# Optimization experiments

Measured on AMD Instinct MI355X. Metric: run time of the kernel, lower is better.

The kernel has to match this reference:

```python
import jax, jax.numpy as jnp
import numpy as np

B, N, D, E, H = 16, 1024, 1024, 4, 16


def setup_inputs() -> dict:
    key = jax.random.key(0)
    k1, k2, k3, k4 = jax.random.split(key, 4)
    return {
        "input_tokens": jax.random.normal(k1, (B, N, D), dtype=jnp.float32),
        "expert_mask": jax.random.randint(k2, (B, N), 0, E, dtype=jnp.int32),
        "qkv_w": jax.random.normal(k3, (3 * D, D), dtype=jnp.float32) * 0.02,
        "proj_w": jax.random.normal(k4, (D, D), dtype=jnp.float32) * 0.02,
        "proj_b": jnp.zeros((D,), dtype=jnp.float32),
    }


def reference(input_tokens, expert_mask, qkv_w, proj_w, proj_b):
    b, n, d = input_tokens.shape
    hd = d // H
    scale = 1.0 / np.sqrt(hd).astype(np.float32)
    # nested expert e uses first d_e = D / 2^(E-1-e) features (expert E-1 = full dim)
    d_tok = d // (2 ** (E - 1 - expert_mask))                     # [B, N]
    feat_mask = (jnp.arange(d)[None, None, :] < d_tok[..., None]).astype(input_tokens.dtype)  # [B, N, D]
    # NestedLinearExpand: slice input features per token (== mask), full 3D output
    x_in = input_tokens * feat_mask
    qkv = jnp.einsum('bnd,fd->bnf', x_in, qkv_w).reshape(b, n, 3, H, hd)
    q, k, v = jnp.moveaxis(qkv, 2, 0)                             # each [B, N, H, hd]
    q = q.transpose(0, 2, 1, 3)                                   # [B, H, N, hd]
    k = k.transpose(0, 2, 1, 3)
    v = v.transpose(0, 2, 1, 3)
    scores = jnp.einsum('bhqd,bhkd->bhqk', q, k) * scale          # [B, H, N, N]
    attn = jax.nn.softmax(scores, axis=-1)
    x = jnp.einsum('bhqk,bhkd->bhqd', attn, v)                    # [B, H, N, hd]
    x = x.transpose(0, 2, 1, 3).reshape(b, n, d)
    # NestedLinearContract: full-dim matmul, only first d_e outputs kept per token
    y = jnp.einsum('bnd,fd->bnf', x, proj_w) + proj_b
    return y * feat_mask
```

## Files before the change

### kernel.cpp

```cpp
#include <hip/hip_runtime.h>
#include <hip/hip_bf16.h>


typedef __bf16 bf16_t;
typedef __bf16 bf16x8 __attribute__((ext_vector_type(8)));
typedef __bf16 bf16x4 __attribute__((ext_vector_type(4)));
typedef float f32x4 __attribute__((ext_vector_type(4)));
typedef float f32x16 __attribute__((ext_vector_type(16)));
typedef int i32x4 __attribute__((ext_vector_type(4)));

typedef __attribute__((address_space(1))) void gvoid;
typedef __attribute__((address_space(3))) void lvoid;

#define MFMA16(a, b, c) __builtin_amdgcn_mfma_f32_16x16x32_bf16((a), (b), (c), 0, 0, 0)
#define MFMA32(a, b, c) __builtin_amdgcn_mfma_f32_32x32x16_bf16((a), (b), (c), 0, 0, 0)
#define GLOAD_LDS16(gsrc, ldst) \
  __builtin_amdgcn_global_load_lds((gvoid*)(gsrc), (lvoid*)(ldst), 16, 0, 0)

#define QSCALE 0.18033688f

__device__ __forceinline__ unsigned cvtpk(float lo, float hi) {
  unsigned r;
  asm("v_cvt_pk_bf16_f32 %0, %1, %2" : "=v"(r) : "v"(lo), "v"(hi));
  return r;
}
__device__ __forceinline__ void pl32swap(unsigned& x, unsigned& y) {
  asm("v_permlane32_swap_b32 %0, %1" : "+v"(x), "+v"(y));
}

__global__ __launch_bounds__(256) void sort_batch(
    const int* __restrict__ em, int* __restrict__ perm, int* __restrict__ ems) {
  __shared__ int cnt[4], base[4], cur[4];
  const int b = blockIdx.x, t = threadIdx.x;
  if (t < 4) cnt[t] = 0;
  __syncthreads();
  int e[4];
#pragma unroll
  for (int i = 0; i < 4; ++i) {
    e[i] = em[b * 1024 + t * 4 + i];
    atomicAdd(&cnt[e[i]], 1);
  }
  __syncthreads();
  if (t == 0) {
    base[0] = 0; base[1] = cnt[0];
    base[2] = cnt[0] + cnt[1]; base[3] = cnt[0] + cnt[1] + cnt[2];
    cur[0] = cur[1] = cur[2] = cur[3] = 0;
  }
  __syncthreads();
#pragma unroll
  for (int i = 0; i < 4; ++i) {
    const int pos = base[e[i]] + atomicAdd(&cur[e[i]], 1);
    perm[b * 1024 + pos] = t * 4 + i;
    ems[b * 1024 + pos] = e[i];
  }
}

__global__ __launch_bounds__(256) void prep_tokens(
    const float* __restrict__ x, const int* __restrict__ perm,
    const int* __restrict__ ems, bf16_t* __restrict__ xq) {
  const int prow = blockIdx.x;
  const int orig = (prow & ~1023) + perm[prow];
  const int dt = 128 << ems[prow];
  const int d = threadIdx.x * 4;
  float4 v = ((const float4*)(x + (size_t)orig * 1024))[threadIdx.x];
  const bool keep = d < dt;
  bf16x4 o;
  o[0] = (bf16_t)(keep ? v.x : 0.f);
  o[1] = (bf16_t)(keep ? v.y : 0.f);
  o[2] = (bf16_t)(keep ? v.z : 0.f);
  o[3] = (bf16_t)(keep ? v.w : 0.f);
  *((bf16x4*)(xq + (size_t)prow * 1024 + d)) = o;
}

__global__ __launch_bounds__(256) void conv_w(
    const float* __restrict__ s, bf16_t* __restrict__ dvec) {
  const int i = blockIdx.x * 256 + threadIdx.x;
  float4 v = ((const float4*)s)[i];
  bf16x4 o;
  o[0] = (bf16_t)v.x; o[1] = (bf16_t)v.y; o[2] = (bf16_t)v.z; o[3] = (bf16_t)v.w;
  ((bf16x4*)dvec)[i] = o;
}

template <int EPI>
__global__ __launch_bounds__(512, 2) void gemm256(
    const bf16_t* __restrict__ A, const bf16_t* __restrict__ Bw, int K,
    const int* __restrict__ perm, const int* __restrict__ ems,
    bf16_t* __restrict__ qo, bf16_t* __restrict__ ko, bf16_t* __restrict__ vto,
    float* __restrict__ yout, const float* __restrict__ bias) {
  __shared__ bf16_t lds[2][32768];
  const int tid = threadIdx.x;
  const int lane = tid & 63, w = tid >> 6;
  const int wm = w >> 2, wn = w & 3;
  const int g = lane >> 4, c16 = lane & 15;

  const int bid = blockIdx.x;
  const int rowbase = (bid & 63) * 256;
  const int colbase = (bid >> 6) * 256;

  const int dtmax = 128 << ems[rowbase + 255];

  if constexpr (EPI == 1) {
    if (colbase >= dtmax) {
      const float4 z = make_float4(0.f, 0.f, 0.f, 0.f);
#pragma unroll
      for (int i = 0; i < 32; ++i) {
        const int idx = i * 512 + tid;
        const int r = idx >> 6, c4 = idx & 63;
        const int orow = ((rowbase + r) & ~1023) + perm[rowbase + r];
        ((float4*)(yout + (size_t)orow * 1024 + colbase))[c4] = z;
      }
      return;
    }
  }

  const int NT = (EPI == 0) ? (dtmax >> 6) : (K >> 6);

  const int trow = tid >> 3;
  const int scol = (((tid & 7) ^ (trow & 7)) << 3);
  const bf16_t* pa = A + (size_t)(rowbase + trow) * K + scol;
  const bf16_t* pb = Bw + (size_t)(colbase + trow) * K + scol;

#define STAGE(j, koff, dst)                                       \
  GLOAD_LDS16(((j) < 4 ? pa + (size_t)((j) * 64) * K              \
                       : pb + (size_t)(((j) - 4) * 64) * K) +     \
                  (koff),                                         \
              (dst) + ((j) * 512 + tid) * 8)

#define LDFRAG(base, R, kk)            \
  (*(const bf16x8*)((base) + (size_t)(R) * 64 + \
                    (((((kk) << 2) + g) ^ (c16 & 7)) << 3)))

  f32x4 acc[8][4] = {};

#pragma unroll
  for (int j = 0; j < 8; ++j) STAGE(j, 0, (bf16_t*)lds[0]);
  asm volatile("s_waitcnt vmcnt(0)" ::: "memory");
  __builtin_amdgcn_s_barrier();

  for (int t = 0; t < NT; ++t) {
    const bf16_t* Lb = lds[t & 1];
    const bf16_t* LbB = Lb + 16384;
    const bool pf = (t + 1) < NT;

    if (pf) {
      bf16_t* Sd = (bf16_t*)lds[(t + 1) & 1];
      const int koff = (t + 1) << 6;
#pragma unroll
      for (int j = 0; j < 8; ++j) STAGE(j, koff, Sd);
    }

    bf16x8 af[4][2], af2[4][2], b0[2][2], b1[2][2];
#pragma unroll
    for (int mi = 0; mi < 4; ++mi)
#pragma unroll
      for (int kk = 0; kk < 2; ++kk)
        af[mi][kk] = LDFRAG(Lb, wm * 128 + mi * 16 + c16, kk);
#pragma unroll
    for (int ni = 0; ni < 2; ++ni)
#pragma unroll
      for (int kk = 0; kk < 2; ++kk)
        b0[ni][kk] = LDFRAG(LbB, wn * 64 + ni * 16 + c16, kk);
#pragma unroll
    for (int mi = 0; mi < 4; ++mi)
#pragma unroll
      for (int ni = 0; ni < 2; ++ni)
#pragma unroll
        for (int kk = 0; kk < 2; ++kk)
          acc[mi][ni] = MFMA16(af[mi][kk], b0[ni][kk], acc[mi][ni]);

#pragma unroll
    for (int ni = 0; ni < 2; ++ni)
#pragma unroll
      for (int kk = 0; kk < 2; ++kk)
        b1[ni][kk] = LDFRAG(LbB, wn * 64 + (ni + 2) * 16 + c16, kk);
#pragma unroll
    for (int mi = 0; mi < 4; ++mi)
#pragma unroll
      for (int ni = 0; ni < 2; ++ni)
#pragma unroll
        for (int kk = 0; kk < 2; ++kk)
          acc[mi][ni + 2] = MFMA16(af[mi][kk], b1[ni][kk], acc[mi][ni + 2]);

#pragma unroll
    for (int mi = 0; mi < 4; ++mi)
#pragma unroll
      for (int kk = 0; kk < 2; ++kk)
        af2[mi][kk] = LDFRAG(Lb, wm * 128 + (mi + 4) * 16 + c16, kk);
#pragma unroll
    for (int mi = 0; mi < 4; ++mi)
#pragma unroll
      for (int ni = 0; ni < 2; ++ni)
#pragma unroll
        for (int kk = 0; kk < 2; ++kk)
          acc[mi + 4][ni] = MFMA16(af2[mi][kk], b0[ni][kk], acc[mi + 4][ni]);

#pragma unroll
    for (int mi = 0; mi < 4; ++mi)
#pragma unroll
      for (int ni = 0; ni < 2; ++ni)
#pragma unroll
        for (int kk = 0; kk < 2; ++kk)
          acc[mi + 4][ni + 2] = MFMA16(af2[mi][kk], b1[ni][kk], acc[mi + 4][ni + 2]);

    if (pf) asm volatile("s_waitcnt vmcnt(0)" ::: "memory");
    __builtin_amdgcn_s_barrier();
  }

  char* epi = (char*)lds;
  if constexpr (EPI == 0) {
    const int s = colbase >> 10;
    const float qs = (s == 0) ? QSCALE : 1.0f;
    if (s < 2) {
#pragma unroll
      for (int mi = 0; mi < 8; ++mi)
#pragma unroll
        for (int ni = 0; ni < 4; ++ni)
#pragma unroll
          for (int j = 0; j < 4; ++j) {
            const int r = wm * 128 + mi * 16 + g * 4 + j;
            const int c = wn * 64 + ni * 16 + c16;
            *(bf16_t*)(epi + r * 512 + 2 * (c ^ (g << 4))) =
                (bf16_t)(acc[mi][ni][j] * qs);
          }
      __builtin_amdgcn_s_barrier();
      bf16_t* const dstbase = (s == 0) ? qo : ko;
#pragma unroll
      for (int it = 0; it < 16; ++it) {
        const int flat = it * 512 + tid;
        const int r = flat >> 5, c0 = (flat & 31) * 8;
        const int gr = (r >> 2) & 3;
        bf16x8 v = *(const bf16x8*)(epi + r * 512 + 2 * (c0 ^ (gr << 4)));
        const int prow = rowbase + r;
        const int bb = prow >> 10, n = prow & 1023;
        const int f = colbase + c0;
        const int h = (f >> 6) & 15, e = f & 63;
        const size_t bh = (size_t)(bb * 16 + h);
        *(bf16x8*)(dstbase + (bh * 1024 + n) * 64 + e) = v;
      }
    } else {
#pragma unroll
      for (int mi = 0; mi < 8; ++mi)
#pragma unroll
        for (int ni = 0; ni < 4; ++ni)
#pragma unroll
          for (int j = 0; j < 4; ++j) {
            const int r = wm * 128 + mi * 16 + g * 4 + j;
            const int c = wn * 64 + ni * 16 + c16;
            *(bf16_t*)(epi + c * 512 + 2 * (r ^ ((c16 >> 2) << 4))) =
                (bf16_t)acc[mi][ni][j];
          }
      __builtin_amdgcn_s_barrier();
      const int bb = rowbase >> 10;
      const int nb = rowbase & 1023;
#pragma unroll
      for (int it = 0; it < 16; ++it) {
        const int flat = it * 512 + tid;
        const int c = flat >> 5, r0 = (flat & 31) * 8;
        const int cc = (c >> 2) & 3;
        bf16x8 v = *(const bf16x8*)(epi + c * 512 + 2 * (r0 ^ (cc << 4)));
        const int f = colbase + c;
        const int h = (f >> 6) & 15, e = f & 63;
        const size_t bh = (size_t)(bb * 16 + h);
        *(bf16x8*)(vto + (bh * 64 + e) * 1024 + nb + r0) = v;
      }
    }
  } else {
#pragma unroll
    for (int p = 0; p < 2; ++p) {
      if (p) __builtin_amdgcn_s_barrier();
      if (wm == p) {
#pragma unroll
        for (int mi = 0; mi < 8; ++mi)
#pragma unroll
          for (int ni = 0; ni < 4; ++ni)
#pragma unroll
            for (int j = 0; j < 4; ++j) {
              const int rl = mi * 16 + g * 4 + j;
              const int c = wn * 64 + ni * 16 + c16;
              *(float*)(epi + rl * 1024 + 4 * (c ^ (g << 4))) = acc[mi][ni][j];
            }
      }
      __builtin_amdgcn_s_barrier();
#pragma unroll
      for (int it = 0; it < 16; ++it) {
        const int flat = it * 512 + tid;
        const int rl = flat >> 6, c0 = (flat & 63) * 4;
        const int gr = (rl >> 2) & 3;
        float4 v = *(const float4*)(epi + rl * 1024 + 4 * (c0 ^ (gr << 4)));
        const int pr = rowbase + p * 128 + rl;
        const int orow = (pr & ~1023) + perm[pr];
        const int dt = 128 << ems[pr];
        const int col = colbase + c0;
        const float4 bia = *(const float4*)(bias + col);
        const bool keep = col < dt;
        float4 o;
        o.x = keep ? v.x + bia.x : 0.f;
        o.y = keep ? v.y + bia.y : 0.f;
        o.z = keep ? v.z + bia.z : 0.f;
        o.w = keep ? v.w + bia.w : 0.f;
        *(float4*)(yout + (size_t)orow * 1024 + col) = o;
      }
    }
  }
#undef STAGE
#undef LDFRAG
}

__global__ __launch_bounds__(512, 2) void attn256(
    const bf16_t* __restrict__ Q, const bf16_t* __restrict__ Kb,
    const bf16_t* __restrict__ VT, bf16_t* __restrict__ X) {
  __shared__ bf16_t Klds[2][8192];
  __shared__ bf16_t Vlds[2][8192];
  const int tid = threadIdx.x;
  const int w = tid >> 6, lane = tid & 63;
  const int k32 = lane & 31, q5 = lane >> 5;
  const int bh = blockIdx.x;
  const int qbase0 = blockIdx.y * 256;
  const int qbase = qbase0 + w * 32;

  const bf16_t* Qbh = Q + (size_t)bh * 65536;
  const bf16_t* Kbh = Kb + (size_t)bh * 65536;
  const bf16_t* Vbh = VT + (size_t)bh * 65536;

  const int ktrow = tid >> 3;
  const int ktslot = (tid & 7) ^ (ktrow & 7);
  const bf16_t* kg = Kbh + (size_t)ktrow * 64 + ktslot * 8;
  const int vtrow = tid >> 4;
  const int vtslot = (tid & 15) ^ (vtrow & 15);
  const bf16_t* vg = Vbh + (size_t)vtrow * 1024 + vtslot * 8;

#define STAGE_KV(b, kt)                                              \
  {                                                                  \
    GLOAD_LDS16(kg + (size_t)(kt) * 64, (bf16_t*)Klds[b] + tid * 8); \
    GLOAD_LDS16(kg + (size_t)(kt) * 64 + 4096,                      \
                (bf16_t*)Klds[b] + 4096 + tid * 8);                  \
    GLOAD_LDS16(vg + (kt), (bf16_t*)Vlds[b] + tid * 8);              \
    GLOAD_LDS16(vg + (kt) + 32768, (bf16_t*)Vlds[b] + 4096 + tid * 8); \
  }

  bf16x8 qf[4];
#pragma unroll
  for (int kc = 0; kc < 4; ++kc)
    qf[kc] = *(const bf16x8*)(Qbh + (size_t)(qbase + k32) * 64 + kc * 16 + q5 * 8);
  asm volatile("" ::"v"(qf[0]), "v"(qf[1]), "v"(qf[2]), "v"(qf[3]));

  const int rswz8 = (k32 & 7) << 4;
  const int rswz16 = (k32 & 15) << 4;

  f32x16 O0 = {}, O1 = {};
  float m = -3.0e38f, lsum = 0.f;

  STAGE_KV(0, 0);

  for (int step = 0; step < 8; ++step) {
    const int buf = step & 1;
    if (step < 7) {
      STAGE_KV(buf ^ 1, (step + 1) * 128);
      asm volatile("s_waitcnt vmcnt(4)" ::: "memory");
    } else {
      asm volatile("s_waitcnt vmcnt(0)" ::: "memory");
    }
    __builtin_amdgcn_s_barrier();

    const char* Vl = (const char*)Vlds[buf];

#pragma unroll
    for (int h = 0; h < 2; ++h) {
      const char* Kl = (const char*)Klds[buf] + h * 8192;

      f32x16 S0 = {}, S1 = {};
#pragma unroll
      for (int kc = 0; kc < 4; ++kc) {
        const int off = k32 * 128 + ((q5 * 16 + kc * 32) ^ rswz8);
        bf16x8 kf0 = *(const bf16x8*)(Kl + off);
        bf16x8 kf1 = *(const bf16x8*)(Kl + off + 4096);
        S0 = MFMA32(kf0, qf[kc], S0);
        S1 = MFMA32(kf1, qf[kc], S1);
      }

      float pm = fmaxf(S0[0], S1[0]);
#pragma unroll
      for (int r = 1; r < 16; ++r) pm = fmaxf(fmaxf(S0[r], S1[r]), pm);
      pm = fmaxf(pm, __shfl_xor(pm, 32));
      if (__any(pm > m + 8.f)) {
        const float mnew = fmaxf(m, pm);
        const float corr = __builtin_amdgcn_exp2f(m - mnew);
        m = mnew;
        lsum *= corr;
        const int ci = __builtin_bit_cast(int, corr);
#pragma unroll
        for (int r = 0; r < 16; ++r) {
          const int qsel = (r & 3) + 8 * (r >> 2) + 4 * q5;
          const float cr = __builtin_bit_cast(
              float, __builtin_amdgcn_ds_bpermute(qsel << 2, ci));
          O0[r] *= cr;
          O1[r] *= cr;
        }
      }
      float ps = 0.f;
#pragma unroll
      for (int r = 0; r < 16; ++r) {
        float p = __builtin_amdgcn_exp2f(S0[r] - m);
        ps += p; S0[r] = p;
        p = __builtin_amdgcn_exp2f(S1[r] - m);
        ps += p; S1[r] = p;
      }
      lsum += ps;

#define MAKE_PA(PV, B0, PA)                            \
  {                                                    \
    unsigned a_ = cvtpk(PV[B0 + 0], PV[B0 + 1]);       \
    unsigned b_ = cvtpk(PV[B0 + 2], PV[B0 + 3]);       \
    unsigned c_ = cvtpk(PV[B0 + 4], PV[B0 + 5]);       \
    unsigned d_ = cvtpk(PV[B0 + 6], PV[B0 + 7]);       \
    pl32swap(a_, c_);                                  \
    pl32swap(b_, d_);                                  \
    i32x4 wv_;                                         \
    wv_[0] = a_; wv_[1] = b_; wv_[2] = c_; wv_[3] = d_; \
    PA = __builtin_bit_cast(bf16x8, wv_);              \
  }
#define PV_STEP(PV, B0, KS)                                         \
  {                                                                 \
    bf16x8 pa;                                                      \
    MAKE_PA(PV, B0, pa);                                            \
    const int voff = k32 * 256 + ((q5 * 16 + (KS) * 32) ^ rswz16);  \
    bf16x8 vf0 = *(const bf16x8*)(Vl + voff);                       \
    bf16x8 vf1 = *(const bf16x8*)(Vl + voff + 8192);                \
    O0 = MFMA32(pa, vf0, O0);                                       \
    O1 = MFMA32(pa, vf1, O1);                                       \
  }
      PV_STEP(S0, 0, h * 4 + 0)
      PV_STEP(S0, 8, h * 4 + 1)
      PV_STEP(S1, 0, h * 4 + 2)
      PV_STEP(S1, 8, h * 4 + 3)
    }

    __builtin_amdgcn_s_barrier();
  }

  lsum += __shfl_xor(lsum, 32);
  const float rinv = 1.f / lsum;
  const int ri = __builtin_bit_cast(int, rinv);
  char* Xs = (char*)Klds;
#pragma unroll
  for (int r = 0; r < 16; ++r) {
    const int qsel = (r & 3) + 8 * (r >> 2) + 4 * q5;
    const float rv = __builtin_bit_cast(
        float, __builtin_amdgcn_ds_bpermute(qsel << 2, ri));
    const int row = w * 32 + qsel;
    const int msk = (row & 7) << 4;
    *(bf16_t*)(Xs + row * 128 + ((2 * k32) ^ msk)) = (bf16_t)(O0[r] * rv);
    *(bf16_t*)(Xs + row * 128 + ((64 + 2 * k32) ^ msk)) = (bf16_t)(O1[r] * rv);
  }
  __builtin_amdgcn_s_barrier();
  const int bb = bh >> 4, h = bh & 15;
  bf16_t* Xb = X + (size_t)bb * 1024 * 1024 + h * 64;
#pragma unroll
  for (int it = 0; it < 4; ++it) {
    const int flat = it * 512 + tid;
    const int row = flat >> 3, ch = flat & 7;
    bf16x8 v = *(const bf16x8*)(Xs + row * 128 + ((ch * 16) ^ ((row & 7) << 4)));
    *(bf16x8*)(Xb + (size_t)(qbase0 + row) * 1024 + ch * 8) = v;
  }
#undef STAGE_KV
#undef MAKE_PA
#undef PV_STEP
}

extern "C" void kernel_launch(void* const* d_in, const int* in_sizes, int n_in,
                              void* d_out, int out_size, void* d_ws,
                              size_t ws_size, hipStream_t stream) {
  const float* x = (const float*)d_in[0];
  const int* em = (const int*)d_in[1];
  const float* qkvw = (const float*)d_in[2];
  const float* projw = (const float*)d_in[3];
  const float* projb = (const float*)d_in[4];
  float* out = (float*)d_out;

  char* ws = (char*)d_ws;
  size_t off = 0;
  bf16_t* xin = (bf16_t*)(ws + off); off += (size_t)16384 * 1024 * 2;
  bf16_t* wq  = (bf16_t*)(ws + off); off += (size_t)3072 * 1024 * 2;
  bf16_t* wp  = (bf16_t*)(ws + off); off += (size_t)1024 * 1024 * 2;
  bf16_t* Qb  = (bf16_t*)(ws + off); off += (size_t)256 * 1024 * 64 * 2;
  bf16_t* Kb  = (bf16_t*)(ws + off); off += (size_t)256 * 1024 * 64 * 2;
  bf16_t* VTb = (bf16_t*)(ws + off); off += (size_t)256 * 64 * 1024 * 2;
  int* perm   = (int*)(ws + off); off += 16384 * 4;
  int* ems    = (int*)(ws + off); off += 16384 * 4;

  sort_batch<<<16, 256, 0, stream>>>(em, perm, ems);

  prep_tokens<<<16384, 256, 0, stream>>>(x, perm, ems, xin);
  conv_w<<<3072, 256, 0, stream>>>(qkvw, wq);
  conv_w<<<1024, 256, 0, stream>>>(projw, wp);

  gemm256<0><<<768, 512, 0, stream>>>(
      xin, wq, 1024, perm, ems, Qb, Kb, VTb, nullptr, nullptr);

  attn256<<<dim3(256, 4), 512, 0, stream>>>(Qb, Kb, VTb, xin);

  gemm256<1><<<256, 512, 0, stream>>>(
      xin, wp, 1024, perm, ems, nullptr, nullptr, nullptr, out, projb);
}
```

Before: 265.3 us.

## Stagger attention half-tile order across waves and raise priority around MFMA blocks

Within the attention kernel, odd waves now process the two K/V half-tiles in reverse order. This spreads LDS bank traffic and lets one wave's softmax overlap another wave's MFMAs. The QK and PV MFMA sections are wrapped in s_setprio to favour matrix issue. The row-max and exp-sum reductions become tree/multi-accumulator forms to shorten dependency chains. All P fragments are packed before the PV MFMAs. Packing them early raises register pressure and reorders the floating-point summation slightly.

After: 275.0 us. 1.04x slower.

```diff
diff --git a/kernel.cpp b/kernel.cpp
--- a/kernel.cpp
+++ b/kernel.cpp
@@ -314,6 +314,7 @@
   const int tid = threadIdx.x;
   const int w = tid >> 6, lane = tid & 63;
   const int k32 = lane & 31, q5 = lane >> 5;
+  const int wp = w & 1;
   const int bh = blockIdx.x;
   const int qbase0 = blockIdx.y * 256;
   const int qbase = qbase0 + w * 32;
@@ -365,10 +366,12 @@
     const char* Vl = (const char*)Vlds[buf];
 
 #pragma unroll
-    for (int h = 0; h < 2; ++h) {
+    for (int hh = 0; hh < 2; ++hh) {
+      const int h = hh ^ wp;
       const char* Kl = (const char*)Klds[buf] + h * 8192;
 
       f32x16 S0 = {}, S1 = {};
+      __builtin_amdgcn_s_setprio(1);
 #pragma unroll
       for (int kc = 0; kc < 4; ++kc) {
         const int off = k32 * 128 + ((q5 * 16 + kc * 32) ^ rswz8);
@@ -377,11 +380,17 @@
         S0 = MFMA32(kf0, qf[kc], S0);
         S1 = MFMA32(kf1, qf[kc], S1);
       }
-
-      float pm = fmaxf(S0[0], S1[0]);
-#pragma unroll
-      for (int r = 1; r < 16; ++r) pm = fmaxf(fmaxf(S0[r], S1[r]), pm);
+      __builtin_amdgcn_s_setprio(0);
+
+      float mx[8];
+#pragma unroll
+      for (int i = 0; i < 8; ++i)
+        mx[i] = fmaxf(fmaxf(S0[i], S0[i + 8]), fmaxf(S1[i], S1[i + 8]));
+#pragma unroll
+      for (int i = 0; i < 4; ++i) mx[i] = fmaxf(mx[i], mx[i + 4]);
+      float pm = fmaxf(fmaxf(mx[0], mx[1]), fmaxf(mx[2], mx[3]));
       pm = fmaxf(pm, __shfl_xor(pm, 32));
+
       if (__any(pm > m + 8.f)) {
         const float mnew = fmaxf(m, pm);
         const float corr = __builtin_amdgcn_exp2f(m - mnew);
@@ -397,15 +406,24 @@
           O1[r] *= cr;
         }
       }
-      float ps = 0.f;
-#pragma unroll
-      for (int r = 0; r < 16; ++r) {
-        float p = __builtin_amdgcn_exp2f(S0[r] - m);
-        ps += p; S0[r] = p;
-        p = __builtin_amdgcn_exp2f(S1[r] - m);
-        ps += p; S1[r] = p;
-      }
-      lsum += ps;
+
+      float ps0 = 0.f, ps1 = 0.f, ps2 = 0.f, ps3 = 0.f;
+#pragma unroll
+      for (int r = 0; r < 4; ++r) {
+        float a0 = __builtin_amdgcn_exp2f(S0[r] - m);
+        float a1 = __builtin_amdgcn_exp2f(S0[r + 4] - m);
+        float a2 = __builtin_amdgcn_exp2f(S0[r + 8] - m);
+        float a3 = __builtin_amdgcn_exp2f(S0[r + 12] - m);
+        S0[r] = a0; S0[r + 4] = a1; S0[r + 8] = a2; S0[r + 12] = a3;
+        ps0 += a0; ps1 += a1; ps2 += a2; ps3 += a3;
+        float b0_ = __builtin_amdgcn_exp2f(S1[r] - m);
+        float b1_ = __builtin_amdgcn_exp2f(S1[r + 4] - m);
+        float b2_ = __builtin_amdgcn_exp2f(S1[r + 8] - m);
+        float b3_ = __builtin_amdgcn_exp2f(S1[r + 12] - m);
+        S1[r] = b0_; S1[r + 4] = b1_; S1[r + 8] = b2_; S1[r + 12] = b3_;
+        ps0 += b0_; ps1 += b1_; ps2 += b2_; ps3 += b3_;
+      }
+      lsum += (ps0 + ps1) + (ps2 + ps3);
 
 #define MAKE_PA(PV, B0, PA)                            \
   {                                                    \
@@ -419,20 +437,26 @@
     wv_[0] = a_; wv_[1] = b_; wv_[2] = c_; wv_[3] = d_; \
     PA = __builtin_bit_cast(bf16x8, wv_);              \
   }
-#define PV_STEP(PV, B0, KS)                                         \
+      bf16x8 pa0, pa1, pa2, pa3;
+      MAKE_PA(S0, 0, pa0);
+      MAKE_PA(S0, 8, pa1);
+      MAKE_PA(S1, 0, pa2);
+      MAKE_PA(S1, 8, pa3);
+
+#define PV_STEP(PA, KS)                                             \
   {                                                                 \
-    bf16x8 pa;                                                      \
-    MAKE_PA(PV, B0, pa);                                            \
     const int voff = k32 * 256 + ((q5 * 16 + (KS) * 32) ^ rswz16);  \
     bf16x8 vf0 = *(const bf16x8*)(Vl + voff);                       \
     bf16x8 vf1 = *(const bf16x8*)(Vl + voff + 8192);                \
-    O0 = MFMA32(pa, vf0, O0);                                       \
-    O1 = MFMA32(pa, vf1, O1);                                       \
-  }
-      PV_STEP(S0, 0, h * 4 + 0)
-      PV_STEP(S0, 8, h * 4 + 1)
-      PV_STEP(S1, 0, h * 4 + 2)
-      PV_STEP(S1, 8, h * 4 + 3)
+    O0 = MFMA32(PA, vf0, O0);                                       \
+    O1 = MFMA32(PA, vf1, O1);                                       \
+  }
+      __builtin_amdgcn_s_setprio(1);
+      PV_STEP(pa0, h * 4 + 0)
+      PV_STEP(pa1, h * 4 + 1)
+      PV_STEP(pa2, h * 4 + 2)
+      PV_STEP(pa3, h * 4 + 3)
+      __builtin_amdgcn_s_setprio(0);
     }
 
     __builtin_amdgcn_s_barrier();
```

## Process two 32-row query tiles per wave in attention to reuse K/V fragments

Applied to the files above, without the earlier changes.

Each attention block now covers 512 query rows instead of 256. Every wave keeps two sets of Q fragments, accumulators and softmax state, so each K and V fragment read from LDS feeds twice as many MFMAs and the K/V global traffic per query is halved. The grid is halved to 512 blocks and launch bounds drop to one block per SIMD group, which raises register pressure and lowers occupancy. Fewer blocks on a large GPU may also leave compute units underused. The output staging buffer is reused in one unified shared array to hold 512 rows.

Result: no change. 260.6 us, median of 2 (-1.8%).

```diff
diff --git a/kernel.cpp b/kernel.cpp
--- a/kernel.cpp
+++ b/kernel.cpp
@@ -306,17 +306,19 @@
 #undef LDFRAG
 }
 
-__global__ __launch_bounds__(512, 2) void attn256(
+__global__ __launch_bounds__(512, 1) void attn256(
     const bf16_t* __restrict__ Q, const bf16_t* __restrict__ Kb,
     const bf16_t* __restrict__ VT, bf16_t* __restrict__ X) {
-  __shared__ bf16_t Klds[2][8192];
-  __shared__ bf16_t Vlds[2][8192];
+  __shared__ bf16_t SH[32768];
+  bf16_t* const Kbuf0 = SH;
+  bf16_t* const Kbuf1 = SH + 8192;
+  bf16_t* const Vbuf0 = SH + 16384;
+  bf16_t* const Vbuf1 = SH + 24576;
   const int tid = threadIdx.x;
   const int w = tid >> 6, lane = tid & 63;
   const int k32 = lane & 31, q5 = lane >> 5;
   const int bh = blockIdx.x;
-  const int qbase0 = blockIdx.y * 256;
-  const int qbase = qbase0 + w * 32;
+  const int qbase0 = blockIdx.y * 512;
 
   const bf16_t* Qbh = Q + (size_t)bh * 65536;
   const bf16_t* Kbh = Kb + (size_t)bh * 65536;
@@ -329,83 +331,96 @@
   const int vtslot = (tid & 15) ^ (vtrow & 15);
   const bf16_t* vg = Vbh + (size_t)vtrow * 1024 + vtslot * 8;
 
-#define STAGE_KV(b, kt)                                              \
-  {                                                                  \
-    GLOAD_LDS16(kg + (size_t)(kt) * 64, (bf16_t*)Klds[b] + tid * 8); \
-    GLOAD_LDS16(kg + (size_t)(kt) * 64 + 4096,                      \
-                (bf16_t*)Klds[b] + 4096 + tid * 8);                  \
-    GLOAD_LDS16(vg + (kt), (bf16_t*)Vlds[b] + tid * 8);              \
-    GLOAD_LDS16(vg + (kt) + 32768, (bf16_t*)Vlds[b] + 4096 + tid * 8); \
-  }
-
-  bf16x8 qf[4];
-#pragma unroll
-  for (int kc = 0; kc < 4; ++kc)
-    qf[kc] = *(const bf16x8*)(Qbh + (size_t)(qbase + k32) * 64 + kc * 16 + q5 * 8);
-  asm volatile("" ::"v"(qf[0]), "v"(qf[1]), "v"(qf[2]), "v"(qf[3]));
+#define STAGE_KV(KD, VD, kt)                                   \
+  {                                                            \
+    GLOAD_LDS16(kg + (size_t)(kt) * 64, (KD) + tid * 8);       \
+    GLOAD_LDS16(kg + (size_t)(kt) * 64 + 4096,                 \
+                (KD) + 4096 + tid * 8);                        \
+    GLOAD_LDS16(vg + (kt), (VD) + tid * 8);                    \
+    GLOAD_LDS16(vg + (kt) + 32768, (VD) + 4096 + tid * 8);     \
+  }
+
+  bf16x8 qf[2][4];
+#pragma unroll
+  for (int t = 0; t < 2; ++t)
+#pragma unroll
+    for (int kc = 0; kc < 4; ++kc)
+      qf[t][kc] = *(const bf16x8*)(Qbh +
+          (size_t)(qbase0 + t * 256 + w * 32 + k32) * 64 + kc * 16 + q5 * 8);
+  asm volatile("" ::"v"(qf[0][0]), "v"(qf[0][1]), "v"(qf[0][2]), "v"(qf[0][3]),
+                   "v"(qf[1][0]), "v"(qf[1][1]), "v"(qf[1][2]), "v"(qf[1][3]));
 
   const int rswz8 = (k32 & 7) << 4;
   const int rswz16 = (k32 & 15) << 4;
 
-  f32x16 O0 = {}, O1 = {};
-  float m = -3.0e38f, lsum = 0.f;
-
-  STAGE_KV(0, 0);
+  f32x16 O0[2] = {}, O1[2] = {};
+  float m[2] = {-3.0e38f, -3.0e38f};
+  float lsum[2] = {0.f, 0.f};
+
+  STAGE_KV(Kbuf0, Vbuf0, 0);
 
   for (int step = 0; step < 8; ++step) {
     const int buf = step & 1;
     if (step < 7) {
-      STAGE_KV(buf ^ 1, (step + 1) * 128);
+      if (buf) { STAGE_KV(Kbuf0, Vbuf0, (step + 1) * 128); }
+      else     { STAGE_KV(Kbuf1, Vbuf1, (step + 1) * 128); }
       asm volatile("s_waitcnt vmcnt(4)" ::: "memory");
     } else {
       asm volatile("s_waitcnt vmcnt(0)" ::: "memory");
     }
     __builtin_amdgcn_s_barrier();
 
-    const char* Vl = (const char*)Vlds[buf];
+    const char* Kbase = (const char*)(buf ? Kbuf1 : Kbuf0);
+    const char* Vl = (const char*)(buf ? Vbuf1 : Vbuf0);
 
 #pragma unroll
     for (int h = 0; h < 2; ++h) {
-      const char* Kl = (const char*)Klds[buf] + h * 8192;
-
-      f32x16 S0 = {}, S1 = {};
+      const char* Kl = Kbase + h * 8192;
+
+      f32x16 S0[2] = {}, S1[2] = {};
 #pragma unroll
       for (int kc = 0; kc < 4; ++kc) {
         const int off = k32 * 128 + ((q5 * 16 + kc * 32) ^ rswz8);
         bf16x8 kf0 = *(const bf16x8*)(Kl + off);
         bf16x8 kf1 = *(const bf16x8*)(Kl + off + 4096);
-        S0 = MFMA32(kf0, qf[kc], S0);
-        S1 = MFMA32(kf1, qf[kc], S1);
-      }
-
-      float pm = fmaxf(S0[0], S1[0]);
-#pragma unroll
-      for (int r = 1; r < 16; ++r) pm = fmaxf(fmaxf(S0[r], S1[r]), pm);
-      pm = fmaxf(pm, __shfl_xor(pm, 32));
-      if (__any(pm > m + 8.f)) {
-        const float mnew = fmaxf(m, pm);
-        const float corr = __builtin_amdgcn_exp2f(m - mnew);
-        m = mnew;
-        lsum *= corr;
-        const int ci = __builtin_bit_cast(int, corr);
+        S0[0] = MFMA32(kf0, qf[0][kc], S0[0]);
+        S1[0] = MFMA32(kf1, qf[0][kc], S1[0]);
+        S0[1] = MFMA32(kf0, qf[1][kc], S0[1]);
+        S1[1] = MFMA32(kf1, qf[1][kc], S1[1]);
+      }
+
+      bf16x8 pa[2][4];
+#pragma unroll
+      for (int t = 0; t < 2; ++t) {
+        float pm = fmaxf(S0[t][0], S1[t][0]);
+#pragma unroll
+        for (int r = 1; r < 16; ++r)
+          pm = fmaxf(pm, fmaxf(S0[t][r], S1[t][r]));
+        pm = fmaxf(pm, __shfl_xor(pm, 32));
+        if (__any(pm > m[t] + 8.f)) {
+          const float mnew = fmaxf(m[t], pm);
+          const float corr = __builtin_amdgcn_exp2f(m[t] - mnew);
+          m[t] = mnew;
+          lsum[t] *= corr;
+          const int ci = __builtin_bit_cast(int, corr);
+#pragma unroll
+          for (int r = 0; r < 16; ++r) {
+            const int qsel = (r & 3) + 8 * (r >> 2) + 4 * q5;
+            const float cr = __builtin_bit_cast(
+                float, __builtin_amdgcn_ds_bpermute(qsel << 2, ci));
+            O0[t][r] *= cr;
+            O1[t][r] *= cr;
+          }
+        }
+        float ps = 0.f;
 #pragma unroll
         for (int r = 0; r < 16; ++r) {
-          const int qsel = (r & 3) + 8 * (r >> 2) + 4 * q5;
-          const float cr = __builtin_bit_cast(
-              float, __builtin_amdgcn_ds_bpermute(qsel << 2, ci));
-          O0[r] *= cr;
-          O1[r] *= cr;
+          float p = __builtin_amdgcn_exp2f(S0[t][r] - m[t]);
+          ps += p; S0[t][r] = p;
+          p = __builtin_amdgcn_exp2f(S1[t][r] - m[t]);
+          ps += p; S1[t][r] = p;
         }
-      }
-      float ps = 0.f;
-#pragma unroll
-      for (int r = 0; r < 16; ++r) {
-        float p = __builtin_amdgcn_exp2f(S0[r] - m);
-        ps += p; S0[r] = p;
-        p = __builtin_amdgcn_exp2f(S1[r] - m);
-        ps += p; S1[r] = p;
-      }
-      lsum += ps;
+        lsum[t] += ps;
 
 #define MAKE_PA(PV, B0, PA)                            \
   {                                                    \
@@ -419,44 +434,51 @@
     wv_[0] = a_; wv_[1] = b_; wv_[2] = c_; wv_[3] = d_; \
     PA = __builtin_bit_cast(bf16x8, wv_);              \
   }
-#define PV_STEP(PV, B0, KS)                                         \
-  {                                                                 \
-    bf16x8 pa;                                                      \
-    MAKE_PA(PV, B0, pa);                                            \
-    const int voff = k32 * 256 + ((q5 * 16 + (KS) * 32) ^ rswz16);  \
-    bf16x8 vf0 = *(const bf16x8*)(Vl + voff);                       \
-    bf16x8 vf1 = *(const bf16x8*)(Vl + voff + 8192);                \
-    O0 = MFMA32(pa, vf0, O0);                                       \
-    O1 = MFMA32(pa, vf1, O1);                                       \
-  }
-      PV_STEP(S0, 0, h * 4 + 0)
-      PV_STEP(S0, 8, h * 4 + 1)
-      PV_STEP(S1, 0, h * 4 + 2)
-      PV_STEP(S1, 8, h * 4 + 3)
+        MAKE_PA(S0[t], 0, pa[t][0]);
+        MAKE_PA(S0[t], 8, pa[t][1]);
+        MAKE_PA(S1[t], 0, pa[t][2]);
+        MAKE_PA(S1[t], 8, pa[t][3]);
+      }
+
+#pragma unroll
+      for (int KS = 0; KS < 4; ++KS) {
+        const int voff = k32 * 256 + ((q5 * 16 + (h * 4 + KS) * 32) ^ rswz16);
+        bf16x8 vf0 = *(const bf16x8*)(Vl + voff);
+        bf16x8 vf1 = *(const bf16x8*)(Vl + voff + 8192);
+        O0[0] = MFMA32(pa[0][KS], vf0, O0[0]);
+        O1[0] = MFMA32(pa[0][KS], vf1, O1[0]);
+        O0[1] = MFMA32(pa[1][KS], vf0, O0[1]);
+        O1[1] = MFMA32(pa[1][KS], vf1, O1[1]);
+      }
     }
 
     __builtin_amdgcn_s_barrier();
   }
 
-  lsum += __shfl_xor(lsum, 32);
-  const float rinv = 1.f / lsum;
-  const int ri = __builtin_bit_cast(int, rinv);
-  char* Xs = (char*)Klds;
-#pragma unroll
-  for (int r = 0; r < 16; ++r) {
-    const int qsel = (r & 3) + 8 * (r >> 2) + 4 * q5;
-    const float rv = __builtin_bit_cast(
-        float, __builtin_amdgcn_ds_bpermute(qsel << 2, ri));
-    const int row = w * 32 + qsel;
-    const int msk = (row & 7) << 4;
-    *(bf16_t*)(Xs + row * 128 + ((2 * k32) ^ msk)) = (bf16_t)(O0[r] * rv);
-    *(bf16_t*)(Xs + row * 128 + ((64 + 2 * k32) ^ msk)) = (bf16_t)(O1[r] * rv);
+  char* Xs = (char*)SH;
+#pragma unroll
+  for (int t = 0; t < 2; ++t) {
+    lsum[t] += __shfl_xor(lsum[t], 32);
+    const float rinv = 1.f / lsum[t];
+    const int ri = __builtin_bit_cast(int, rinv);
+#pragma unroll
+    for (int r = 0; r < 16; ++r) {
+      const int qsel = (r & 3) + 8 * (r >> 2) + 4 * q5;
+      const float rv = __builtin_bit_cast(
+          float, __builtin_amdgcn_ds_bpermute(qsel << 2, ri));
+      const int row = t * 256 + w * 32 + qsel;
+      const int msk = (row & 7) << 4;
+      *(bf16_t*)(Xs + row * 128 + ((2 * k32) ^ msk)) =
+          (bf16_t)(O0[t][r] * rv);
+      *(bf16_t*)(Xs + row * 128 + ((64 + 2 * k32) ^ msk)) =
+          (bf16_t)(O1[t][r] * rv);
+    }
   }
   __builtin_amdgcn_s_barrier();
-  const int bb = bh >> 4, h = bh & 15;
-  bf16_t* Xb = X + (size_t)bb * 1024 * 1024 + h * 64;
-#pragma unroll
-  for (int it = 0; it < 4; ++it) {
+  const int bb = bh >> 4, hh = bh & 15;
+  bf16_t* Xb = X + (size_t)bb * 1024 * 1024 + hh * 64;
+#pragma unroll
+  for (int it = 0; it < 8; ++it) {
     const int flat = it * 512 + tid;
     const int row = flat >> 3, ch = flat & 7;
     bf16x8 v = *(const bf16x8*)(Xs + row * 128 + ((ch * 16) ^ ((row & 7) << 4)));
@@ -464,7 +486,6 @@
   }
 #undef STAGE_KV
 #undef MAKE_PA
-#undef PV_STEP
 }
 
 extern "C" void kernel_launch(void* const* d_in, const int* in_sizes, int n_in,
@@ -497,7 +518,7 @@
   gemm256<0><<<768, 512, 0, stream>>>(
       xin, wq, 1024, perm, ems, Qb, Kb, VTb, nullptr, nullptr);
 
-  attn256<<<dim3(256, 4), 512, 0, stream>>>(Qb, Kb, VTb, xin);
+  attn256<<<dim3(256, 2), 512, 0, stream>>>(Qb, Kb, VTb, xin);
 
   gemm256<1><<<256, 512, 0, stream>>>(
       xin, wp, 1024, perm, ems, nullptr, nullptr, nullptr, out, projb);
```
